# Optimization experiments

Measured on AMD Instinct MI355X. Metric: run time of the kernel, lower is better.

The kernel has to match this reference:

```python
import jax, jax.numpy as jnp
import numpy as np

N_NODES = 50000
N_EDGES = 800000
N_GRAPHS = 2048
IN_DIM = 128
HID = 256
N_LAYERS = 4
BN_EPS = 1e-5


def setup_inputs() -> dict:
    key = jax.random.key(0)
    ks = jax.random.split(key, 12)
    x = jax.random.normal(ks[0], (N_NODES, IN_DIM), dtype=jnp.float32)
    edge_index = jax.random.randint(ks[1], (2, N_EDGES), 0, N_NODES, dtype=jnp.int64)
    batch = jnp.sort(jax.random.randint(ks[2], (N_NODES,), 0, N_GRAPHS, dtype=jnp.int64))
    convW0 = jax.random.normal(ks[3], (IN_DIM, HID), dtype=jnp.float32) * (IN_DIM ** -0.5)
    convWs = jax.random.normal(ks[4], (N_LAYERS - 1, HID, HID), dtype=jnp.float32) * (HID ** -0.5)
    convB = jnp.zeros((N_LAYERS, HID), dtype=jnp.float32)
    bn_gamma = jnp.ones((N_LAYERS, HID), dtype=jnp.float32)
    bn_beta = jnp.zeros((N_LAYERS, HID), dtype=jnp.float32)
    bn_mean = jnp.zeros((N_LAYERS, HID), dtype=jnp.float32)
    bn_var = jax.random.uniform(ks[5], (N_LAYERS, HID), dtype=jnp.float32, minval=0.5, maxval=1.5)
    lin1W = jax.random.normal(ks[6], (HID, HID // 2), dtype=jnp.float32) * (HID ** -0.5)
    lin1b = jnp.zeros((HID // 2,), dtype=jnp.float32)
    lin2W = jax.random.normal(ks[7], (HID // 2, 1), dtype=jnp.float32) * ((HID // 2) ** -0.5)
    lin2b = jnp.zeros((1,), dtype=jnp.float32)
    return dict(x=x, edge_index=edge_index, batch=batch, convW0=convW0, convWs=convWs,
                convB=convB, bn_gamma=bn_gamma, bn_beta=bn_beta, bn_mean=bn_mean,
                bn_var=bn_var, lin1W=lin1W, lin1b=lin1b, lin2W=lin2W, lin2b=lin2b)


def reference(x, edge_index, batch, convW0, convWs, convB, bn_gamma, bn_beta,
              bn_mean, bn_var, lin1W, lin1b, lin2W, lin2b):
    N = x.shape[0]
    src, dst = edge_index[0], edge_index[1]
    # degree with self-loops (PyG GCNConv default add_self_loops=True)
    deg = jnp.zeros((N,), dtype=x.dtype).at[dst].add(1.0) + 1.0
    dinv = deg ** -0.5
    enorm = (dinv[src] * dinv[dst])[:, None]      # [E,1]
    self_norm = (1.0 / deg)[:, None]              # [N,1] self-loop weight

    def gcn_conv(h, W, b):
        h = h @ W                                 # [N,H]
        agg = jax.ops.segment_sum(h[src] * enorm, dst, num_segments=N)
        return agg + h * self_norm + b

    Ws = [convW0] + [convWs[i] for i in range(convWs.shape[0])]
    for l in range(N_LAYERS):
        x = gcn_conv(x, Ws[l], convB[l])
        # eval-mode BatchNorm1d
        x = (x - bn_mean[l]) * jax.lax.rsqrt(bn_var[l] + BN_EPS) * bn_gamma[l] + bn_beta[l]
        x = jax.nn.relu(x)
        # dropout: identity in eval mode

    # global_mean_pool over graph ids
    sums = jax.ops.segment_sum(x, batch, num_segments=N_GRAPHS)      # [G,H]
    cnts = jax.ops.segment_sum(jnp.ones((N,), x.dtype), batch, num_segments=N_GRAPHS)
    pooled = sums / jnp.maximum(cnts, 1.0)[:, None]

    h = jax.nn.relu(pooled @ lin1W + lin1b)
    out = (h @ lin2W + lin2b).squeeze(-1)          # [G]
    return out
```

## Files before the change

kernel.cpp:

```cpp
#include <hip/hip_runtime.h>

#define N_NODES 50000
#define N_EDGES 800000
#define N_GRAPHS 2048
#define IN_DIM 128
#define HID 256
#define N_LAYERS 4
#define BN_EPS 1e-5f
#define NBIN 128
#define WSCALE 64.0f

typedef unsigned short ushort_t;
typedef float f32x4 __attribute__((ext_vector_type(4)));
typedef unsigned int u32x4 __attribute__((ext_vector_type(4)));
typedef _Float16 f16x8 __attribute__((ext_vector_type(8)));
typedef _Float16 f16x4 __attribute__((ext_vector_type(4)));

__device__ __forceinline__ void gl_lds16(const ushort_t* g, ushort_t* l) {
    __builtin_amdgcn_global_load_lds(
        (const __attribute__((address_space(1))) void*)g,
        (__attribute__((address_space(3))) void*)l, 16, 0, 0);
}

__global__ void k_deg(const int* __restrict__ dst, int* __restrict__ degi, int E) {
    int e = blockIdx.x * blockDim.x + threadIdx.x;
    if (e < E) atomicAdd(&degi[dst[e]], 1);
}

__global__ __launch_bounds__(256) void k_nodeprep(const int* __restrict__ degi,
                                                  float* __restrict__ dinv,
                                                  float* __restrict__ selfn,
                                                  int* __restrict__ bins, int N) {
    __shared__ int lbin[NBIN];
    int t = threadIdx.x;
    if (t < NBIN) lbin[t] = 0;
    __syncthreads();
    int n = blockIdx.x * 256 + t;
    if (n < N) {
        int dg = degi[n];
        float d = 1.0f + (float)dg;
        dinv[n] = 1.0f / sqrtf(d);
        selfn[n] = 1.0f / d;
        atomicAdd(&lbin[min(dg, NBIN - 1)], 1);
    }
    __syncthreads();
    if (t < NBIN && lbin[t] > 0) atomicAdd(&bins[t], lbin[t]);
}

__global__ void k_binscan(const int* __restrict__ bins, int* __restrict__ binstart,
                          int* __restrict__ bincur, int* __restrict__ edgebase) {
    if (threadIdx.x == 0) {
        int run = 0, erun = 0;
        for (int d = 0; d < NBIN; ++d) {
            binstart[d] = run;
            bincur[d] = run;
            edgebase[d] = erun;
            run += bins[d];
            erun += bins[d] * d;
        }
    }
}

__global__ __launch_bounds__(256) void k_assign(const int* __restrict__ degi,
                                                const int* __restrict__ binstart,
                                                const int* __restrict__ edgebase,
                                                const int* __restrict__ bins,
                                                int* __restrict__ bincur,
                                                int* __restrict__ perm, int* __restrict__ invperm,
                                                int2* __restrict__ meta, int* __restrict__ cursor,
                                                int N) {
    __shared__ int lbin[NBIN];
    __shared__ int lbase[NBIN];
    int t = threadIdx.x;
    if (t < NBIN) lbin[t] = 0;
    __syncthreads();
    int n = blockIdx.x * 256 + t;
    int d = 0, lrank = 0;
    if (n < N) {
        d = min(degi[n], NBIN - 1);
        lrank = atomicAdd(&lbin[d], 1);
    }
    __syncthreads();
    if (t < NBIN && lbin[t] > 0) lbase[t] = atomicAdd(&bincur[t], lbin[t]);
    __syncthreads();
    if (n < N) {
        int slot = lbase[d] + lrank;
        perm[slot] = n;
        invperm[n] = slot;
        int2 m;
        m.x = edgebase[d] + (slot - binstart[d]);
        m.y = bins[d] | (d << 20);
        meta[slot] = m;
        cursor[slot] = 0;
    }
}

__global__ void k_fill(const int* __restrict__ src, const int* __restrict__ dst,
                       const float* __restrict__ dinv, const int* __restrict__ invperm,
                       const int2* __restrict__ meta, int* __restrict__ cursor,
                       int2* __restrict__ edata, int E) {
    int e = blockIdx.x * blockDim.x + threadIdx.x;
    if (e >= E) return;
    int s = src[e], d = dst[e];
    int slot = invperm[d];
    int2 m = meta[slot];
    int j = atomicAdd(&cursor[slot], 1);
    int pos = m.x + j * (m.y & 0xFFFFF);
    int2 v;
    v.x = s;
    v.y = __float_as_int(dinv[s] * dinv[d]);
    edata[pos] = v;
}

__global__ void k_bounds(const int* __restrict__ batch, int* __restrict__ gstart,
                         int* __restrict__ gend, int N) {
    int n = blockIdx.x * blockDim.x + threadIdx.x;
    if (n >= N) return;
    int g = batch[n];
    if (n == 0 || batch[n - 1] != g) gstart[g] = n;
    if (n == N - 1 || batch[n + 1] != g) gend[g] = n + 1;
}

__global__ __launch_bounds__(256) void k_prep(const float* __restrict__ gamma,
                                              const float* __restrict__ beta,
                                              const float* __restrict__ mean,
                                              const float* __restrict__ var,
                                              const float* __restrict__ bias,
                                              const float* __restrict__ W0,
                                              const float* __restrict__ Ws,
                                              const float* __restrict__ x,
                                              float* __restrict__ scale,
                                              float* __restrict__ shift,
                                              _Float16* __restrict__ Wh,
                                              _Float16* __restrict__ Wl,
                                              _Float16* __restrict__ X16) {
    int id = blockIdx.x * 256 + threadIdx.x;
    if (id < N_LAYERS * HID) {
        float s = gamma[id] * rsqrtf(var[id] + BN_EPS);
        scale[id] = s / WSCALE;
        shift[id] = beta[id] + (bias[id] - mean[id]) * s;
        return;
    }
    id -= N_LAYERS * HID;
    const int WT = 128 * 256 + 3 * 256 * 256;
    if (id < WT) {
        float v;
        if (id < 32768) {
            int n = id >> 7, k = id & 127;
            v = W0[k * 256 + n];
        } else {
            int t = id - 32768;
            int l = t >> 16;
            int r = t & 65535;
            int n = r >> 8, k = r & 255;
            v = Ws[l * 65536 + k * 256 + n];
        }
        v *= WSCALE;
        _Float16 h = (_Float16)v;
        Wh[id] = h;
        Wl[id] = (_Float16)(v - (float)h);
        return;
    }
    id -= WT;
    const int total4 = N_NODES * IN_DIM / 4;
    if (id < total4) {
        float4 v = ((const float4*)x)[id];
        int n = id >> 5;
        int c0 = (id & 31) * 4;
        f16x4 o;
        o.x = (_Float16)v.x; o.y = (_Float16)v.y; o.z = (_Float16)v.z; o.w = (_Float16)v.w;
        *(f16x4*)(X16 + (size_t)(c0 >> 5) * (N_NODES * 32) + (size_t)n * 32 + (c0 & 31)) = o;
    }
}

__global__ __launch_bounds__(256) void k_gemm(const _Float16* __restrict__ A,
                                              const _Float16* __restrict__ Wh,
                                              const _Float16* __restrict__ Wl,
                                              const float* __restrict__ bnscale,
                                              const float* __restrict__ bnshift,
                                              _Float16* __restrict__ X16, int K) {
    __shared__ _Float16 sm[3 * 128 * 32];
    _Float16* tA  = sm;
    _Float16* tWh = sm + 4096;
    _Float16* tWl = sm + 8192;

    int tid = threadIdx.x;
    int lane = tid & 63;
    int w = tid >> 6;
    int wrow = w & 1, wcol = w >> 1;
    int row0 = blockIdx.x * 128;
    int col0 = blockIdx.y * 128;

    int srow = lane >> 2;
    int sch = lane & 3;

    f32x4 acc[4][4] = {};
    int m = lane & 15, q = lane >> 4;

    for (int k0 = 0; k0 < K; k0 += 32) {
        #pragma unroll
        for (int ii = 0; ii < 6; ++ii) {
            int G = w * 6 + ii;
            int mat = G >> 3;
            int grp = G & 7;
            const _Float16* gs = (mat == 0) ? A : (mat == 1) ? Wh : Wl;
            _Float16* ld = sm + mat * 4096;
            int rb = (mat == 0) ? row0 : col0;
            int rl = (mat == 0) ? N_NODES : (col0 + 128);
            int r = grp * 16 + srow;
            int grow = rb + r;
            int gch = sch ^ (r & 3);
            if (grow < rl)
                gl_lds16((const ushort_t*)(gs + (size_t)grow * K + k0 + gch * 8),
                         (ushort_t*)(ld + grp * 512));
        }
        __syncthreads();

        f16x8 af[4], whf[4], wlf[4];
        #pragma unroll
        for (int r = 0; r < 4; ++r) {
            int rr = wrow * 64 + r * 16 + m;
            int off = rr * 32 + ((q ^ (rr & 3)) << 3);
            af[r] = *(const f16x8*)(tA + off);
        }
        #pragma unroll
        for (int c = 0; c < 4; ++c) {
            int nn = wcol * 64 + c * 16 + m;
            int off = nn * 32 + ((q ^ (nn & 3)) << 3);
            whf[c] = *(const f16x8*)(tWh + off);
            wlf[c] = *(const f16x8*)(tWl + off);
        }
        #pragma unroll
        for (int r = 0; r < 4; ++r)
            #pragma unroll
            for (int c = 0; c < 4; ++c) {
                acc[r][c] = __builtin_amdgcn_mfma_f32_16x16x32_f16(af[r], whf[c], acc[r][c], 0, 0, 0);
                acc[r][c] = __builtin_amdgcn_mfma_f32_16x16x32_f16(af[r], wlf[c], acc[r][c], 0, 0, 0);
            }
        __syncthreads();
    }

    #pragma unroll
    for (int r = 0; r < 4; ++r) {
        int mrow = row0 + wrow * 64 + r * 16 + (lane >> 4) * 4;
        #pragma unroll
        for (int c = 0; c < 4; ++c) {
            int n = col0 + wcol * 64 + c * 16 + (lane & 15);
            float sc = bnscale[n];
            float sh = bnshift[n];
            f32x4 v = acc[r][c];
            _Float16* base = X16 + (size_t)(n >> 5) * (N_NODES * 32) + (n & 31);
            #pragma unroll
            for (int g = 0; g < 4; ++g)
                if (mrow + g < N_NODES)
                    base[(size_t)(mrow + g) * 32] =
                        (_Float16)fmaxf(fmaf(v[g], sc, sh), 0.f);
        }
    }
}

#define GNB 782

__global__ __launch_bounds__(256) void k_gather(const _Float16* __restrict__ Xc,
                                                const int2* __restrict__ meta,
                                                const int2* __restrict__ edata,
                                                const int* __restrict__ perm,
                                                const float* __restrict__ selfn,
                                                _Float16* __restrict__ A,
                                                int K, int cshift) {
    int bid = blockIdx.x;
    int chunk = bid & ((1 << cshift) - 1);
    int nb = bid >> cshift;
    const _Float16* Hc = Xc + (size_t)chunk * (N_NODES * 32);
    int slot = nb * 64 + (threadIdx.x >> 2);
    if (slot >= N_NODES) return;
    int node = perm[slot];
    int2 m = meta[slot];
    int q8 = (threadIdx.x & 3) * 8;

    int stride = m.y & 0xFFFFF;
    int deg = m.y >> 20;
    const int2* ep = edata + m.x;
    float sn = selfn[node];

    float acc[8];
    {
        f16x8 hv = *(const f16x8*)(Hc + (size_t)node * 32 + q8);
        #pragma unroll
        for (int i = 0; i < 8; ++i) acc[i] = (float)hv[i] * sn;
    }
    int j = 0;
    for (; j + 3 < deg; j += 4) {
        int2 e0 = ep[(size_t)(j + 0) * stride];
        int2 e1 = ep[(size_t)(j + 1) * stride];
        int2 e2 = ep[(size_t)(j + 2) * stride];
        int2 e3 = ep[(size_t)(j + 3) * stride];
        f16x8 a0 = *(const f16x8*)(Hc + (size_t)e0.x * 32 + q8);
        f16x8 a1 = *(const f16x8*)(Hc + (size_t)e1.x * 32 + q8);
        f16x8 a2 = *(const f16x8*)(Hc + (size_t)e2.x * 32 + q8);
        f16x8 a3 = *(const f16x8*)(Hc + (size_t)e3.x * 32 + q8);
        float w0 = __int_as_float(e0.y);
        float w1 = __int_as_float(e1.y);
        float w2 = __int_as_float(e2.y);
        float w3 = __int_as_float(e3.y);
        #pragma unroll
        for (int i = 0; i < 8; ++i) {
            acc[i] = fmaf((float)a0[i], w0, acc[i]);
            acc[i] = fmaf((float)a1[i], w1, acc[i]);
            acc[i] = fmaf((float)a2[i], w2, acc[i]);
            acc[i] = fmaf((float)a3[i], w3, acc[i]);
        }
    }
    for (; j < deg; ++j) {
        int2 e0 = ep[(size_t)j * stride];
        f16x8 a0 = *(const f16x8*)(Hc + (size_t)e0.x * 32 + q8);
        float w0 = __int_as_float(e0.y);
        #pragma unroll
        for (int i = 0; i < 8; ++i) acc[i] = fmaf((float)a0[i], w0, acc[i]);
    }

    f16x8 o;
    #pragma unroll
    for (int i = 0; i < 8; ++i) o[i] = (_Float16)acc[i];
    u32x4 uv = *(u32x4*)&o;
    __builtin_nontemporal_store(uv, (u32x4*)(A + (size_t)node * K + chunk * 32 + q8));
}

__global__ __launch_bounds__(128) void k_poolmlp(const _Float16* __restrict__ X16,
                                                 const int* __restrict__ gstart,
                                                 const int* __restrict__ gend,
                                                 const float* __restrict__ W1,
                                                 const float* __restrict__ b1,
                                                 const float* __restrict__ W2,
                                                 const float* __restrict__ b2,
                                                 float* __restrict__ out) {
    __shared__ float prow[HID];
    __shared__ float hred[2];
    int g = blockIdx.x;
    int s = gstart[g], e = gend[g];
    int j = threadIdx.x;
    const _Float16* p0 = X16 + (size_t)(j >> 5) * (N_NODES * 32) + (j & 31);
    const _Float16* p1 = X16 + (size_t)((j >> 5) + 4) * (N_NODES * 32) + (j & 31);
    float a0 = 0.f, a1 = 0.f;
    for (int n = s; n < e; ++n) {
        a0 += (float)p0[(size_t)n * 32];
        a1 += (float)p1[(size_t)n * 32];
    }
    float inv = 1.0f / fmaxf((float)(e - s), 1.0f);
    prow[j] = a0 * inv;
    prow[j + 128] = a1 * inv;
    __syncthreads();
    float acc = 0.f;
    #pragma unroll 8
    for (int k = 0; k < HID; ++k) acc += prow[k] * W1[k * 128 + j];
    float h = fmaxf(acc + b1[j], 0.f);
    float p = h * W2[j];
    #pragma unroll
    for (int off = 32; off > 0; off >>= 1) p += __shfl_down(p, off, 64);
    if ((j & 63) == 0) hred[j >> 6] = p;
    __syncthreads();
    if (j == 0) out[g] = hred[0] + hred[1] + b2[0];
}

extern "C" void kernel_launch(void* const* d_in, const int* in_sizes, int n_in,
                              void* d_out, int out_size, void* d_ws, size_t ws_size,
                              hipStream_t stream) {
    const float* x      = (const float*)d_in[0];
    const int*   ei     = (const int*)d_in[1];
    const int*   batch  = (const int*)d_in[2];
    const float* convW0 = (const float*)d_in[3];
    const float* convWs = (const float*)d_in[4];
    const float* convB  = (const float*)d_in[5];
    const float* gamma  = (const float*)d_in[6];
    const float* beta   = (const float*)d_in[7];
    const float* mean   = (const float*)d_in[8];
    const float* var    = (const float*)d_in[9];
    const float* lin1W  = (const float*)d_in[10];
    const float* lin1b  = (const float*)d_in[11];
    const float* lin2W  = (const float*)d_in[12];
    const float* lin2b  = (const float*)d_in[13];
    float* out = (float*)d_out;

    const int* src = ei;
    const int* dst = ei + N_EDGES;

    const int WTOT = 128 * 256 + 3 * 256 * 256;

    char* wsb = (char*)d_ws;
    _Float16* x16a = (_Float16*)wsb;
    _Float16* x16b = x16a + (size_t)N_NODES * HID;
    _Float16* Ab   = x16b + (size_t)N_NODES * HID;
    _Float16* Wh16 = Ab + (size_t)N_NODES * HID;
    _Float16* Wl16 = Wh16 + WTOT;
    float* dinv    = (float*)(Wl16 + WTOT);
    float* selfn   = dinv + N_NODES;
    float* bnscale = selfn + N_NODES;
    float* bnshift = bnscale + N_LAYERS * HID;
    int*   degi    = (int*)(bnshift + N_LAYERS * HID);
    int*   bins    = degi + N_NODES;
    int*   gstart  = bins + NBIN;
    int*   gend    = gstart + N_GRAPHS;
    int*   binstart= gend + N_GRAPHS;
    int*   bincur  = binstart + NBIN;
    int*   edgebase= bincur + NBIN;
    int*   cursor  = edgebase + NBIN;
    int*   perm    = cursor + N_NODES;
    int*   invperm = perm + N_NODES;
    int2*  meta    = (int2*)(invperm + N_NODES);
    int2*  edata   = meta + N_NODES;

    hipMemsetAsync(degi, 0, (size_t)(N_NODES + NBIN + 2 * N_GRAPHS) * 4, stream);

    k_deg<<<(N_EDGES + 255) / 256, 256, 0, stream>>>(dst, degi, N_EDGES);
    k_nodeprep<<<(N_NODES + 255) / 256, 256, 0, stream>>>(degi, dinv, selfn, bins, N_NODES);
    k_binscan<<<1, 64, 0, stream>>>(bins, binstart, bincur, edgebase);
    k_assign<<<(N_NODES + 255) / 256, 256, 0, stream>>>(degi, binstart, edgebase, bins, bincur,
                                                        perm, invperm, meta, cursor, N_NODES);
    k_fill<<<(N_EDGES + 255) / 256, 256, 0, stream>>>(src, dst, dinv, invperm, meta, cursor,
                                                      edata, N_EDGES);
    k_bounds<<<(N_NODES + 255) / 256, 256, 0, stream>>>(batch, gstart, gend, N_NODES);

    const int PREP_TOT = N_LAYERS * HID + WTOT + N_NODES * IN_DIM / 4;
    k_prep<<<(PREP_TOT + 255) / 256, 256, 0, stream>>>(gamma, beta, mean, var, convB,
                                                       convW0, convWs, x,
                                                       bnscale, bnshift, Wh16, Wl16, x16a);

    dim3 gg((N_NODES + 127) / 128, 2);
    _Float16* cur = x16a;
    for (int l = 0; l < N_LAYERS; ++l) {
        int K = (l == 0) ? IN_DIM : HID;
        int nchunk = K / 32;
        int cshift = (l == 0) ? 2 : 3;
        size_t woff = (l == 0) ? 0 : (size_t)(32768 + (l - 1) * 65536);
        k_gather<<<nchunk * GNB, 256, 0, stream>>>(cur, meta, edata, perm, selfn,
                                                   Ab, K, cshift);
        _Float16* nxt = (cur == x16a) ? x16b : x16a;
        k_gemm<<<gg, 256, 0, stream>>>(Ab, Wh16 + woff, Wl16 + woff,
                                       bnscale + l * HID, bnshift + l * HID, nxt, K);
        cur = nxt;
    }

    k_poolmlp<<<N_GRAPHS, 128, 0, stream>>>(cur, gstart, gend, lin1W, lin1b, lin2W, lin2b, out);
}
```

Before: 506.3 us.

## Pack edge records into 32 bits, widen gather unroll, parallelize bin scan

```diff
diff --git a/kernel.cpp b/kernel.cpp
--- a/kernel.cpp
+++ b/kernel.cpp
@@ -49,16 +49,21 @@
 
 __global__ void k_binscan(const int* __restrict__ bins, int* __restrict__ binstart,
                           int* __restrict__ bincur, int* __restrict__ edgebase) {
-    if (threadIdx.x == 0) {
-        int run = 0, erun = 0;
-        for (int d = 0; d < NBIN; ++d) {
-            binstart[d] = run;
-            bincur[d] = run;
-            edgebase[d] = erun;
-            run += bins[d];
-            erun += bins[d] * d;
-        }
-    }
+    int t = threadIdx.x & 63;
+    int d0 = 2 * t, d1 = 2 * t + 1;
+    int a = bins[d0], b = bins[d1];
+    int ea = a * d0, eb = b * d1;
+    int s = a + b, es = ea + eb;
+    int ps = s, pe = es;
+    #pragma unroll
+    for (int off = 1; off < 64; off <<= 1) {
+        int u = __shfl_up(ps, off, 64);
+        int v = __shfl_up(pe, off, 64);
+        if (t >= off) { ps += u; pe += v; }
+    }
+    int exs = ps - s, exe = pe - es;
+    binstart[d0] = exs;     bincur[d0] = exs;     edgebase[d0] = exe;
+    binstart[d1] = exs + a; bincur[d1] = exs + a; edgebase[d1] = exe + ea;
 }
 
 __global__ __launch_bounds__(256) void k_assign(const int* __restrict__ degi,
@@ -98,7 +103,7 @@
 __global__ void k_fill(const int* __restrict__ src, const int* __restrict__ dst,
                        const float* __restrict__ dinv, const int* __restrict__ invperm,
                        const int2* __restrict__ meta, int* __restrict__ cursor,
-                       int2* __restrict__ edata, int E) {
+                       unsigned int* __restrict__ edata, int E) {
     int e = blockIdx.x * blockDim.x + threadIdx.x;
     if (e >= E) return;
     int s = src[e], d = dst[e];
@@ -106,10 +111,10 @@
     int2 m = meta[slot];
     int j = atomicAdd(&cursor[slot], 1);
     int pos = m.x + j * (m.y & 0xFFFFF);
-    int2 v;
-    v.x = s;
-    v.y = __float_as_int(dinv[s] * dinv[d]);
-    edata[pos] = v;
+    _Float16 hw = (_Float16)(dinv[s] * dinv[d]);
+    unsigned int p = ((unsigned int)__builtin_bit_cast(unsigned short, hw) << 16) |
+                     (unsigned int)s;
+    edata[pos] = p;
 }
 
 __global__ void k_bounds(const int* __restrict__ batch, int* __restrict__ gstart,
@@ -263,7 +268,7 @@
 
 __global__ __launch_bounds__(256) void k_gather(const _Float16* __restrict__ Xc,
                                                 const int2* __restrict__ meta,
-                                                const int2* __restrict__ edata,
+                                                const unsigned int* __restrict__ edata,
                                                 const int* __restrict__ perm,
                                                 const float* __restrict__ selfn,
                                                 _Float16* __restrict__ A,
@@ -280,7 +285,7 @@
 
     int stride = m.y & 0xFFFFF;
     int deg = m.y >> 20;
-    const int2* ep = edata + m.x;
+    const unsigned int* ep = edata + m.x;
     float sn = selfn[node];
 
     float acc[8];
@@ -289,32 +294,45 @@
         #pragma unroll
         for (int i = 0; i < 8; ++i) acc[i] = (float)hv[i] * sn;
     }
+
     int j = 0;
-    for (; j + 3 < deg; j += 4) {
-        int2 e0 = ep[(size_t)(j + 0) * stride];
-        int2 e1 = ep[(size_t)(j + 1) * stride];
-        int2 e2 = ep[(size_t)(j + 2) * stride];
-        int2 e3 = ep[(size_t)(j + 3) * stride];
-        f16x8 a0 = *(const f16x8*)(Hc + (size_t)e0.x * 32 + q8);
-        f16x8 a1 = *(const f16x8*)(Hc + (size_t)e1.x * 32 + q8);
-        f16x8 a2 = *(const f16x8*)(Hc + (size_t)e2.x * 32 + q8);
-        f16x8 a3 = *(const f16x8*)(Hc + (size_t)e3.x * 32 + q8);
-        float w0 = __int_as_float(e0.y);
-        float w1 = __int_as_float(e1.y);
-        float w2 = __int_as_float(e2.y);
-        float w3 = __int_as_float(e3.y);
+    for (; j + 7 < deg; j += 8) {
+        unsigned int e[8];
+        #pragma unroll
+        for (int i = 0; i < 8; ++i)
+            e[i] = __builtin_nontemporal_load(&ep[(size_t)(j + i) * stride]);
+        f16x8 a[8];
+        #pragma unroll
+        for (int i = 0; i < 8; ++i)
+            a[i] = *(const f16x8*)(Hc + (size_t)(e[i] & 0xFFFFu) * 32 + q8);
         #pragma unroll
         for (int i = 0; i < 8; ++i) {
-            acc[i] = fmaf((float)a0[i], w0, acc[i]);
-            acc[i] = fmaf((float)a1[i], w1, acc[i]);
-            acc[i] = fmaf((float)a2[i], w2, acc[i]);
-            acc[i] = fmaf((float)a3[i], w3, acc[i]);
-        }
+            float w = (float)__builtin_bit_cast(_Float16, (unsigned short)(e[i] >> 16));
+            #pragma unroll
+            for (int c = 0; c < 8; ++c) acc[c] = fmaf((float)a[i][c], w, acc[c]);
+        }
+    }
+    if (j + 3 < deg) {
+        unsigned int e[4];
+        #pragma unroll
+        for (int i = 0; i < 4; ++i)
+            e[i] = __builtin_nontemporal_load(&ep[(size_t)(j + i) * stride]);
+        f16x8 a[4];
+        #pragma unroll
+        for (int i = 0; i < 4; ++i)
+            a[i] = *(const f16x8*)(Hc + (size_t)(e[i] & 0xFFFFu) * 32 + q8);
+        #pragma unroll
+        for (int i = 0; i < 4; ++i) {
+            float w = (float)__builtin_bit_cast(_Float16, (unsigned short)(e[i] >> 16));
+            #pragma unroll
+            for (int c = 0; c < 8; ++c) acc[c] = fmaf((float)a[i][c], w, acc[c]);
+        }
+        j += 4;
     }
     for (; j < deg; ++j) {
-        int2 e0 = ep[(size_t)j * stride];
-        f16x8 a0 = *(const f16x8*)(Hc + (size_t)e0.x * 32 + q8);
-        float w0 = __int_as_float(e0.y);
+        unsigned int e0 = __builtin_nontemporal_load(&ep[(size_t)j * stride]);
+        f16x8 a0 = *(const f16x8*)(Hc + (size_t)(e0 & 0xFFFFu) * 32 + q8);
+        float w0 = (float)__builtin_bit_cast(_Float16, (unsigned short)(e0 >> 16));
         #pragma unroll
         for (int i = 0; i < 8; ++i) acc[i] = fmaf((float)a0[i], w0, acc[i]);
     }
@@ -407,7 +425,7 @@
     int*   perm    = cursor + N_NODES;
     int*   invperm = perm + N_NODES;
     int2*  meta    = (int2*)(invperm + N_NODES);
-    int2*  edata   = meta + N_NODES;
+    unsigned int* edata = (unsigned int*)(meta + N_NODES);
 
     hipMemsetAsync(degi, 0, (size_t)(N_NODES + NBIN + 2 * N_GRAPHS) * 4, stream);
 
```

Measured after the change: 560.0 us. 1.11x slower.
